# Optimization experiments

Hardware: AMD Instinct MI355X
Metric: run time of the kernel (lower is better)

The kernel has to match this reference:

```python
import jax, jax.numpy as jnp
import numpy as np


def setup_inputs() -> dict:
    key = jax.random.key(0)
    ks = jax.random.split(key, 7)
    IN, OUT, B = 8192, 8192, 256
    return {
        "x": jax.random.normal(ks[0], (B, IN), dtype=jnp.float32),
        "mu_weights": jax.random.normal(ks[1], (OUT, IN), dtype=jnp.float32) * 0.02,
        "rho_weights": jax.random.normal(ks[2], (OUT, IN), dtype=jnp.float32) * 0.1 - 3.0,
        "mu_bias": jax.random.normal(ks[3], (OUT,), dtype=jnp.float32) * 0.02,
        "rho_bias": jax.random.normal(ks[4], (OUT,), dtype=jnp.float32) * 0.1 - 3.0,
        "eps_w": jax.random.normal(ks[5], (OUT, IN), dtype=jnp.float32),
        "eps_b": jax.random.normal(ks[6], (OUT,), dtype=jnp.float32),
    }


def reference(x, mu_weights, rho_weights, mu_bias, rho_bias, eps_w, eps_b):
    # sigma = log(1 + exp(rho))  (softplus); W = mu + sigma * eps
    sigma_w = jnp.log1p(jnp.exp(rho_weights))
    W = mu_weights + sigma_w * eps_w            # [out, in]
    out = jnp.einsum("bi,oi->bo", x, W)          # x @ W.T -> [b, out]
    sigma_b = jnp.log1p(jnp.exp(rho_bias))
    b = mu_bias + sigma_b * eps_b                # [out]
    return out + b
```

## Files before the change

### kernel.cpp

```cpp
#include <hip/hip_runtime.h>

typedef _Float16 f16;
typedef _Float16 f16x8 __attribute__((ext_vector_type(8)));
typedef float f32x4 __attribute__((ext_vector_type(4)));

#define IN_DIM  8192
#define OUT_DIM 8192
#define BATCH   256
#define BK      32
#define BN      128
#define NSPLIT  4
#define KSPL    (IN_DIM / NSPLIT)
#define NSTEP   (KSPL / BK)

__device__ __forceinline__ float softplus_f(float r) {
    return __logf(1.0f + __expf(r));
}

#define ISSUE(S, A0a,A0b,A1a,A1b,M0,M1,R0,R1,E0,E1) do {                     \
    const int o_ = (S) * BK;                                                 \
    A0a = *(const f32x4*)(xp0 + o_);   A0b = *(const f32x4*)(xp0 + o_ + 4);  \
    A1a = *(const f32x4*)(xp1 + o_);   A1b = *(const f32x4*)(xp1 + o_ + 4);  \
    M0  = *(const f32x4*)(mup + o_);   M1  = *(const f32x4*)(mup + o_ + 4);  \
    R0  = *(const f32x4*)(rhp + o_);   R1  = *(const f32x4*)(rhp + o_ + 4);  \
    E0  = *(const f32x4*)(epp + o_);   E1  = *(const f32x4*)(epp + o_ + 4);  \
} while (0)

#define COMMIT(BUF, A0a,A0b,A1a,A1b,M0,M1,R0,R1,E0,E1) do {                  \
    f16x8 av0_, av1_, wv_;                                                   \
    _Pragma("unroll")                                                        \
    for (int q_ = 0; q_ < 4; ++q_) {                                         \
        av0_[q_]   = (f16)A0a[q_];  av0_[4+q_] = (f16)A0b[q_];               \
        av1_[q_]   = (f16)A1a[q_];  av1_[4+q_] = (f16)A1b[q_];               \
        wv_[q_]   = (f16)(M0[q_] + softplus_f(R0[q_]) * E0[q_]);             \
        wv_[4+q_] = (f16)(M1[q_] + softplus_f(R1[q_]) * E1[q_]);             \
    }                                                                        \
    *(f16x8*)&sm[BUF][a_st0] = av0_;                                         \
    *(f16x8*)&sm[BUF][a_st1] = av1_;                                         \
    *(f16x8*)&sm[BUF][b_st]  = wv_;                                          \
} while (0)

#define MSTEP(BUF) do {                                                      \
    f16x8 af_[4], bf_[4];                                                    \
    const int sl_ = lane >> 4;                                               \
    _Pragma("unroll")                                                        \
    for (int i_ = 0; i_ < 4; ++i_) {                                         \
        const int ar_ = wm * 64 + i_ * 16 + (lane & 15);                     \
        af_[i_] = *(const f16x8*)&sm[BUF][ar_ * BK + ((sl_ ^ (ar_ & 3)) << 3)]; \
        const int br_ = wn * 64 + i_ * 16 + (lane & 15);                     \
        bf_[i_] = *(const f16x8*)&sm[BUF][BATCH * BK + br_ * BK + ((sl_ ^ (br_ & 3)) << 3)]; \
    }                                                                        \
    _Pragma("unroll")                                                        \
    for (int i_ = 0; i_ < 4; ++i_)                                           \
        _Pragma("unroll")                                                    \
        for (int j_ = 0; j_ < 4; ++j_)                                       \
            acc[i_][j_] = __builtin_amdgcn_mfma_f32_16x16x32_f16(            \
                af_[i_], bf_[j_], acc[i_][j_], 0, 0, 0);                     \
} while (0)

#define BARRIER() do {                                                       \
    asm volatile("s_waitcnt lgkmcnt(0)" ::: "memory");                       \
    __builtin_amdgcn_s_barrier();                                            \
} while (0)

__global__ __launch_bounds__(512, 2)
void vl_main(const float* __restrict__ x,
             const float* __restrict__ muw,
             const float* __restrict__ rhow,
             const float* __restrict__ epsw,
             const float* __restrict__ mub,
             const float* __restrict__ rhob,
             const float* __restrict__ epsb,
             float* __restrict__ out)
{
    __shared__ __align__(16) f16 sm[2][BATCH * BK + BN * BK];

    const int t    = threadIdx.x;
    const int lane = t & 63;
    const int wid  = t >> 6;
    const int wm   = wid >> 1;
    const int wn   = wid & 1;

    const int bx = blockIdx.x;
    const int x7 = bx & 7;
    const int sk = x7 >> 1;
    const int nb = (x7 & 1) * 32 + (bx >> 3);
    const int k_base = sk * KSPL;
    const int n_base = nb * BN;

    const int slot = t & 3;
    const int row  = t >> 2;

    const float* xp0 = x + (size_t)row * IN_DIM + k_base + slot * 8;
    const float* xp1 = xp0 + (size_t)128 * IN_DIM;
    const size_t woff = (size_t)(n_base + row) * IN_DIM + k_base + slot * 8;
    const float* mup = muw  + woff;
    const float* rhp = rhow + woff;
    const float* epp = epsw + woff;

    const int a_sw  = (slot ^ (row & 3)) << 3;
    const int a_st0 = row * BK + a_sw;
    const int a_st1 = (row + 128) * BK + a_sw;
    const int b_st  = BATCH * BK + row * BK + a_sw;

    f32x4 acc[4][4];
#pragma unroll
    for (int i = 0; i < 4; ++i)
#pragma unroll
        for (int j = 0; j < 4; ++j)
            acc[i][j] = (f32x4){0.f, 0.f, 0.f, 0.f};

    f32x4 A0a0,A0b0,A1a0,A1b0,M00,M10,R00,R10,E00,E10;
    f32x4 A0a1,A0b1,A1a1,A1b1,M01,M11,R01,R11,E01,E11;

    ISSUE(0, A0a0,A0b0,A1a0,A1b0,M00,M10,R00,R10,E00,E10);
    ISSUE(1, A0a1,A0b1,A1a1,A1b1,M01,M11,R01,R11,E01,E11);
    COMMIT(0, A0a0,A0b0,A1a0,A1b0,M00,M10,R00,R10,E00,E10);
    BARRIER();

    for (int s = 0; s < NSTEP; s += 2) {
        if (s + 2 < NSTEP) ISSUE(s + 2, A0a0,A0b0,A1a0,A1b0,M00,M10,R00,R10,E00,E10);
        MSTEP(0);
        COMMIT(1, A0a1,A0b1,A1a1,A1b1,M01,M11,R01,R11,E01,E11);
        BARRIER();
        if (s + 3 < NSTEP) ISSUE(s + 3, A0a1,A0b1,A1a1,A1b1,M01,M11,R01,R11,E01,E11);
        MSTEP(1);
        if (s + 2 < NSTEP) COMMIT(0, A0a0,A0b0,A1a0,A1b0,M00,M10,R00,R10,E00,E10);
        BARRIER();
    }

    float bias[4] = {0.f, 0.f, 0.f, 0.f};
    if (sk == 0) {
#pragma unroll
        for (int j = 0; j < 4; ++j) {
            const int c = n_base + wn * 64 + j * 16 + (lane & 15);
            bias[j] = mub[c] + softplus_f(rhob[c]) * epsb[c];
        }
    }
#pragma unroll
    for (int i = 0; i < 4; ++i) {
        const int r = wm * 64 + i * 16 + ((lane >> 4) << 2);
#pragma unroll
        for (int j = 0; j < 4; ++j) {
            const int c = n_base + wn * 64 + j * 16 + (lane & 15);
            float* po = out + (size_t)r * OUT_DIM + c;
#pragma unroll
            for (int q = 0; q < 4; ++q)
                atomicAdd(po + (size_t)q * OUT_DIM, acc[i][j][q] + bias[j]);
        }
    }
}

extern "C" void kernel_launch(void* const* d_in, const int* in_sizes, int n_in,
                              void* d_out, int out_size, void* d_ws, size_t ws_size,
                              hipStream_t stream) {
    (void)in_sizes; (void)n_in; (void)d_ws; (void)ws_size;
    const float* x    = (const float*)d_in[0];
    const float* muw  = (const float*)d_in[1];
    const float* rhow = (const float*)d_in[2];
    const float* mub  = (const float*)d_in[3];
    const float* rhob = (const float*)d_in[4];
    const float* epsw = (const float*)d_in[5];
    const float* epsb = (const float*)d_in[6];
    float* out = (float*)d_out;

    hipMemsetAsync(out, 0, (size_t)out_size * sizeof(float), stream);
    vl_main<<<dim3(256), dim3(512), 0, stream>>>(x, muw, rhow, epsw,
                                                 mub, rhob, epsb, out);
}
```

Before: 214.0 us.

## Load x fragments directly into registers and keep only W in LDS

Activation tiles are no longer staged through shared memory. Each wave loads its x rows straight from global memory in MFMA fragment layout, converts them to fp16 in registers, and prefetches one step ahead. Shared memory now holds only the generated weight tile, with a new swizzle, and the last barrier of the loop is skipped. This is meant to cut LDS traffic, LDS footprint and barrier cost. In exchange, x is read redundantly by the two waves that share a row range, with less coalesced 32-byte segments per row, and register pressure goes up.

```diff
diff --git a/kernel.cpp b/kernel.cpp
--- a/kernel.cpp
+++ b/kernel.cpp
@@ -17,45 +17,56 @@
     return __logf(1.0f + __expf(r));
 }
 
-#define ISSUE(S, A0a,A0b,A1a,A1b,M0,M1,R0,R1,E0,E1) do {                     \
+#define ISSUE_W(S, Ma,Mb,Ra,Rb,Ea,Eb) do {                                   \
     const int o_ = (S) * BK;                                                 \
-    A0a = *(const f32x4*)(xp0 + o_);   A0b = *(const f32x4*)(xp0 + o_ + 4);  \
-    A1a = *(const f32x4*)(xp1 + o_);   A1b = *(const f32x4*)(xp1 + o_ + 4);  \
-    M0  = *(const f32x4*)(mup + o_);   M1  = *(const f32x4*)(mup + o_ + 4);  \
-    R0  = *(const f32x4*)(rhp + o_);   R1  = *(const f32x4*)(rhp + o_ + 4);  \
-    E0  = *(const f32x4*)(epp + o_);   E1  = *(const f32x4*)(epp + o_ + 4);  \
+    Ma = *(const f32x4*)(mup + o_);   Mb = *(const f32x4*)(mup + o_ + 4);    \
+    Ra = *(const f32x4*)(rhp + o_);   Rb = *(const f32x4*)(rhp + o_ + 4);    \
+    Ea = *(const f32x4*)(epp + o_);   Eb = *(const f32x4*)(epp + o_ + 4);    \
 } while (0)
 
-#define COMMIT(BUF, A0a,A0b,A1a,A1b,M0,M1,R0,R1,E0,E1) do {                  \
-    f16x8 av0_, av1_, wv_;                                                   \
+#define COMMIT_W(BUF, Ma,Mb,Ra,Rb,Ea,Eb) do {                                \
+    f16x8 wv_;                                                               \
     _Pragma("unroll")                                                        \
     for (int q_ = 0; q_ < 4; ++q_) {                                         \
-        av0_[q_]   = (f16)A0a[q_];  av0_[4+q_] = (f16)A0b[q_];               \
-        av1_[q_]   = (f16)A1a[q_];  av1_[4+q_] = (f16)A1b[q_];               \
-        wv_[q_]   = (f16)(M0[q_] + softplus_f(R0[q_]) * E0[q_]);             \
-        wv_[4+q_] = (f16)(M1[q_] + softplus_f(R1[q_]) * E1[q_]);             \
+        wv_[q_]   = (f16)(Ma[q_] + softplus_f(Ra[q_]) * Ea[q_]);             \
+        wv_[4+q_] = (f16)(Mb[q_] + softplus_f(Rb[q_]) * Eb[q_]);             \
     }                                                                        \
-    *(f16x8*)&sm[BUF][a_st0] = av0_;                                         \
-    *(f16x8*)&sm[BUF][a_st1] = av1_;                                         \
-    *(f16x8*)&sm[BUF][b_st]  = wv_;                                          \
+    *(f16x8*)&sm[BUF][b_st] = wv_;                                           \
+} while (0)
+
+#define ISSUE_A(S) do {                                                      \
+    const int o_ = (S) * BK;                                                 \
+    Ap0 = *(const f32x4*)(xa0 + o_);  Ap1 = *(const f32x4*)(xa0 + o_ + 4);   \
+    Ap2 = *(const f32x4*)(xa1 + o_);  Ap3 = *(const f32x4*)(xa1 + o_ + 4);   \
+    Ap4 = *(const f32x4*)(xa2 + o_);  Ap5 = *(const f32x4*)(xa2 + o_ + 4);   \
+    Ap6 = *(const f32x4*)(xa3 + o_);  Ap7 = *(const f32x4*)(xa3 + o_ + 4);   \
+} while (0)
+
+#define CVT_A() do {                                                         \
+    _Pragma("unroll")                                                        \
+    for (int q_ = 0; q_ < 4; ++q_) {                                         \
+        af0[q_] = (f16)Ap0[q_];  af0[4+q_] = (f16)Ap1[q_];                   \
+        af1[q_] = (f16)Ap2[q_];  af1[4+q_] = (f16)Ap3[q_];                   \
+        af2[q_] = (f16)Ap4[q_];  af2[4+q_] = (f16)Ap5[q_];                   \
+        af3[q_] = (f16)Ap6[q_];  af3[4+q_] = (f16)Ap7[q_];                   \
+    }                                                                        \
 } while (0)
 
 #define MSTEP(BUF) do {                                                      \
-    f16x8 af_[4], bf_[4];                                                    \
-    const int sl_ = lane >> 4;                                               \
+    f16x8 bf_[4];                                                            \
     _Pragma("unroll")                                                        \
-    for (int i_ = 0; i_ < 4; ++i_) {                                         \
-        const int ar_ = wm * 64 + i_ * 16 + (lane & 15);                     \
-        af_[i_] = *(const f16x8*)&sm[BUF][ar_ * BK + ((sl_ ^ (ar_ & 3)) << 3)]; \
-        const int br_ = wn * 64 + i_ * 16 + (lane & 15);                     \
-        bf_[i_] = *(const f16x8*)&sm[BUF][BATCH * BK + br_ * BK + ((sl_ ^ (br_ & 3)) << 3)]; \
+    for (int j_ = 0; j_ < 4; ++j_) {                                         \
+        const int br_ = wn * 64 + j_ * 16 + (lane & 15);                     \
+        bf_[j_] = *(const f16x8*)&sm[BUF][br_ * BK +                         \
+                    (((lane >> 4) ^ ((br_ >> 1) & 3)) << 3)];                \
     }                                                                        \
     _Pragma("unroll")                                                        \
-    for (int i_ = 0; i_ < 4; ++i_)                                           \
-        _Pragma("unroll")                                                    \
-        for (int j_ = 0; j_ < 4; ++j_)                                       \
-            acc[i_][j_] = __builtin_amdgcn_mfma_f32_16x16x32_f16(            \
-                af_[i_], bf_[j_], acc[i_][j_], 0, 0, 0);                     \
+    for (int j_ = 0; j_ < 4; ++j_) {                                         \
+        acc[0][j_] = __builtin_amdgcn_mfma_f32_16x16x32_f16(af0, bf_[j_], acc[0][j_], 0, 0, 0); \
+        acc[1][j_] = __builtin_amdgcn_mfma_f32_16x16x32_f16(af1, bf_[j_], acc[1][j_], 0, 0, 0); \
+        acc[2][j_] = __builtin_amdgcn_mfma_f32_16x16x32_f16(af2, bf_[j_], acc[2][j_], 0, 0, 0); \
+        acc[3][j_] = __builtin_amdgcn_mfma_f32_16x16x32_f16(af3, bf_[j_], acc[3][j_], 0, 0, 0); \
+    }                                                                        \
 } while (0)
 
 #define BARRIER() do {                                                       \
@@ -73,7 +84,7 @@
              const float* __restrict__ epsb,
              float* __restrict__ out)
 {
-    __shared__ __align__(16) f16 sm[2][BATCH * BK + BN * BK];
+    __shared__ __align__(16) f16 sm[2][BN * BK];
 
     const int t    = threadIdx.x;
     const int lane = t & 63;
@@ -90,18 +101,18 @@
 
     const int slot = t & 3;
     const int row  = t >> 2;
-
-    const float* xp0 = x + (size_t)row * IN_DIM + k_base + slot * 8;
-    const float* xp1 = xp0 + (size_t)128 * IN_DIM;
     const size_t woff = (size_t)(n_base + row) * IN_DIM + k_base + slot * 8;
     const float* mup = muw  + woff;
     const float* rhp = rhow + woff;
     const float* epp = epsw + woff;
 
-    const int a_sw  = (slot ^ (row & 3)) << 3;
-    const int a_st0 = row * BK + a_sw;
-    const int a_st1 = (row + 128) * BK + a_sw;
-    const int b_st  = BATCH * BK + row * BK + a_sw;
+    const int b_st = row * BK + ((slot ^ ((row >> 1) & 3)) << 3);
+
+    const int kf = (lane >> 4) * 8;
+    const float* xa0 = x + (size_t)(wm * 64 +  0 + (lane & 15)) * IN_DIM + k_base + kf;
+    const float* xa1 = x + (size_t)(wm * 64 + 16 + (lane & 15)) * IN_DIM + k_base + kf;
+    const float* xa2 = x + (size_t)(wm * 64 + 32 + (lane & 15)) * IN_DIM + k_base + kf;
+    const float* xa3 = x + (size_t)(wm * 64 + 48 + (lane & 15)) * IN_DIM + k_base + kf;
 
     f32x4 acc[4][4];
 #pragma unroll
@@ -110,23 +121,32 @@
         for (int j = 0; j < 4; ++j)
             acc[i][j] = (f32x4){0.f, 0.f, 0.f, 0.f};
 
-    f32x4 A0a0,A0b0,A1a0,A1b0,M00,M10,R00,R10,E00,E10;
-    f32x4 A0a1,A0b1,A1a1,A1b1,M01,M11,R01,R11,E01,E11;
+    f32x4 Ap0, Ap1, Ap2, Ap3, Ap4, Ap5, Ap6, Ap7;
+    f32x4 M0a, M0b, R0a, R0b, E0a, E0b;
+    f32x4 M1a, M1b, R1a, R1b, E1a, E1b;
+    f16x8 af0, af1, af2, af3;
 
-    ISSUE(0, A0a0,A0b0,A1a0,A1b0,M00,M10,R00,R10,E00,E10);
-    ISSUE(1, A0a1,A0b1,A1a1,A1b1,M01,M11,R01,R11,E01,E11);
-    COMMIT(0, A0a0,A0b0,A1a0,A1b0,M00,M10,R00,R10,E00,E10);
+    ISSUE_A(0);
+    ISSUE_W(0, M0a, M0b, R0a, R0b, E0a, E0b);
+    ISSUE_W(1, M1a, M1b, R1a, R1b, E1a, E1b);
+    COMMIT_W(0, M0a, M0b, R0a, R0b, E0a, E0b);
     BARRIER();
 
     for (int s = 0; s < NSTEP; s += 2) {
-        if (s + 2 < NSTEP) ISSUE(s + 2, A0a0,A0b0,A1a0,A1b0,M00,M10,R00,R10,E00,E10);
+        CVT_A();
+        ISSUE_A(s + 1);
+        if (s + 2 < NSTEP) ISSUE_W(s + 2, M0a, M0b, R0a, R0b, E0a, E0b);
         MSTEP(0);
-        COMMIT(1, A0a1,A0b1,A1a1,A1b1,M01,M11,R01,R11,E01,E11);
+        COMMIT_W(1, M1a, M1b, R1a, R1b, E1a, E1b);
         BARRIER();
-        if (s + 3 < NSTEP) ISSUE(s + 3, A0a1,A0b1,A1a1,A1b1,M01,M11,R01,R11,E01,E11);
+        CVT_A();
+        if (s + 2 < NSTEP) ISSUE_A(s + 2);
+        if (s + 3 < NSTEP) ISSUE_W(s + 3, M1a, M1b, R1a, R1b, E1a, E1b);
         MSTEP(1);
-        if (s + 2 < NSTEP) COMMIT(0, A0a0,A0b0,A1a0,A1b0,M00,M10,R00,R10,E00,E10);
-        BARRIER();
+        if (s + 2 < NSTEP) {
+            COMMIT_W(0, M0a, M0b, R0a, R0b, E0a, E0b);
+            BARRIER();
+        }
     }
 
     float bias[4] = {0.f, 0.f, 0.f, 0.f};
```

After: 259.5 us. +21.3%, slower.

## Deepen K-tile to 64 with inline-asm loads and manual vmcnt pipelining

Applied to the files above, without the earlier changes.

Doubles the K step per stage from 32 to 64 and issues global loads through inline `global_load_dwordx4` asm. Explicit `s_waitcnt vmcnt` and sched barriers control when the weight and activation registers are consumed, so the x and weight streams are prefetched a stage ahead. The x tile moves to a single-buffered LDS region with a wider XOR swizzle, while the weight tile stays double-buffered. The aim is to hide HBM latency better and halve the loop-iteration overhead, at the cost of more registers, extra barriers per iteration, and fragile hand-counted wait thresholds.

```diff
diff --git a/kernel.cpp b/kernel.cpp
--- a/kernel.cpp
+++ b/kernel.cpp
@@ -6,56 +6,83 @@
 
 #define IN_DIM  8192
 #define OUT_DIM 8192
-#define BATCH   256
-#define BK      32
-#define BN      128
 #define NSPLIT  4
 #define KSPL    (IN_DIM / NSPLIT)
-#define NSTEP   (KSPL / BK)
+#define BKM     64
+#define NM      (KSPL / BKM)
 
 __device__ __forceinline__ float softplus_f(float r) {
     return __logf(1.0f + __expf(r));
 }
 
-#define ISSUE(S, A0a,A0b,A1a,A1b,M0,M1,R0,R1,E0,E1) do {                     \
-    const int o_ = (S) * BK;                                                 \
-    A0a = *(const f32x4*)(xp0 + o_);   A0b = *(const f32x4*)(xp0 + o_ + 4);  \
-    A1a = *(const f32x4*)(xp1 + o_);   A1b = *(const f32x4*)(xp1 + o_ + 4);  \
-    M0  = *(const f32x4*)(mup + o_);   M1  = *(const f32x4*)(mup + o_ + 4);  \
-    R0  = *(const f32x4*)(rhp + o_);   R1  = *(const f32x4*)(rhp + o_ + 4);  \
-    E0  = *(const f32x4*)(epp + o_);   E1  = *(const f32x4*)(epp + o_ + 4);  \
-} while (0)
-
-#define COMMIT(BUF, A0a,A0b,A1a,A1b,M0,M1,R0,R1,E0,E1) do {                  \
-    f16x8 av0_, av1_, wv_;                                                   \
+#define GLD16(dst, p, LIT) \
+    asm volatile("global_load_dwordx4 %0, %1, off offset:" LIT \
+                 : "=&v"(dst) : "v"(p))
+
+#define SCHED0() __builtin_amdgcn_sched_barrier(0)
+
+#define ISSUE_W(M0,M1,M2,M3,R0,R1,R2,R3,E0,E1,E2,E3, S) do {                 \
+    const float* pm_ = mup + (size_t)(S) * BKM;                              \
+    const float* pr_ = rhp + (size_t)(S) * BKM;                              \
+    const float* pe_ = epp + (size_t)(S) * BKM;                              \
+    GLD16(M0, pm_, "0");  GLD16(M1, pm_, "16");                              \
+    GLD16(M2, pm_, "32"); GLD16(M3, pm_, "48");                              \
+    GLD16(R0, pr_, "0");  GLD16(R1, pr_, "16");                              \
+    GLD16(R2, pr_, "32"); GLD16(R3, pr_, "48");                              \
+    GLD16(E0, pe_, "0");  GLD16(E1, pe_, "16");                              \
+    GLD16(E2, pe_, "32"); GLD16(E3, pe_, "48");                              \
+} while (0)
+
+#define ISSUE_A(S) do {                                                      \
+    const float* pa_ = xap + (size_t)(S) * BKM;                              \
+    GLD16(Aa, pa_, "0");   GLD16(Ab, pa_, "16");                             \
+    GLD16(Ac, pa_, "32");  GLD16(Ad, pa_, "48");                             \
+    GLD16(Ae, pa_, "64");  GLD16(Af, pa_, "80");                             \
+    GLD16(Ag, pa_, "96");  GLD16(Ah, pa_, "112");                            \
+} while (0)
+
+#define COMMIT_W(BUF, M0,M1,M2,M3,R0,R1,R2,R3,E0,E1,E2,E3) do {              \
+    f16x8 w0_, w1_;                                                          \
     _Pragma("unroll")                                                        \
     for (int q_ = 0; q_ < 4; ++q_) {                                         \
-        av0_[q_]   = (f16)A0a[q_];  av0_[4+q_] = (f16)A0b[q_];               \
-        av1_[q_]   = (f16)A1a[q_];  av1_[4+q_] = (f16)A1b[q_];               \
-        wv_[q_]   = (f16)(M0[q_] + softplus_f(R0[q_]) * E0[q_]);             \
-        wv_[4+q_] = (f16)(M1[q_] + softplus_f(R1[q_]) * E1[q_]);             \
+        w0_[q_]   = (f16)(M0[q_] + softplus_f(R0[q_]) * E0[q_]);             \
+        w0_[4+q_] = (f16)(M1[q_] + softplus_f(R1[q_]) * E1[q_]);             \
+        w1_[q_]   = (f16)(M2[q_] + softplus_f(R2[q_]) * E2[q_]);             \
+        w1_[4+q_] = (f16)(M3[q_] + softplus_f(R3[q_]) * E3[q_]);             \
     }                                                                        \
-    *(f16x8*)&sm[BUF][a_st0] = av0_;                                         \
-    *(f16x8*)&sm[BUF][a_st1] = av1_;                                         \
-    *(f16x8*)&sm[BUF][b_st]  = wv_;                                          \
-} while (0)
-
-#define MSTEP(BUF) do {                                                      \
-    f16x8 af_[4], bf_[4];                                                    \
-    const int sl_ = lane >> 4;                                               \
+    *(f16x8*)&smW[BUF][ws0] = w0_;                                           \
+    *(f16x8*)&smW[BUF][ws1] = w1_;                                           \
+} while (0)
+
+#define COMMIT_A() do {                                                      \
+    f16x8 a0_, a1_, a2_, a3_;                                                \
+    _Pragma("unroll")                                                        \
+    for (int q_ = 0; q_ < 4; ++q_) {                                         \
+        a0_[q_] = (f16)Aa[q_];  a0_[4+q_] = (f16)Ab[q_];                     \
+        a1_[q_] = (f16)Ac[q_];  a1_[4+q_] = (f16)Ad[q_];                     \
+        a2_[q_] = (f16)Ae[q_];  a2_[4+q_] = (f16)Af[q_];                     \
+        a3_[q_] = (f16)Ag[q_];  a3_[4+q_] = (f16)Ah[q_];                     \
+    }                                                                        \
+    *(f16x8*)&smA[as0] = a0_;  *(f16x8*)&smA[as1] = a1_;                     \
+    *(f16x8*)&smA[as2] = a2_;  *(f16x8*)&smA[as3] = a3_;                     \
+} while (0)
+
+#define MSTEP(B, HH) do {                                                    \
+    const int ko_ = (HH) * 4 + (lane >> 4);                                  \
+    const int rr_ = lane & 15;                                               \
+    const int xw_ = (ko_ ^ (rr_ & 7)) << 3;                                  \
+    f16x8 bf_[4];                                                            \
+    _Pragma("unroll")                                                        \
+    for (int j_ = 0; j_ < 4; ++j_)                                           \
+        bf_[j_] = *(const f16x8*)&smW[B][(wn*64 + j_*16 + rr_)*BKM + xw_];   \
     _Pragma("unroll")                                                        \
     for (int i_ = 0; i_ < 4; ++i_) {                                         \
-        const int ar_ = wm * 64 + i_ * 16 + (lane & 15);                     \
-        af_[i_] = *(const f16x8*)&sm[BUF][ar_ * BK + ((sl_ ^ (ar_ & 3)) << 3)]; \
-        const int br_ = wn * 64 + i_ * 16 + (lane & 15);                     \
-        bf_[i_] = *(const f16x8*)&sm[BUF][BATCH * BK + br_ * BK + ((sl_ ^ (br_ & 3)) << 3)]; \
-    }                                                                        \
-    _Pragma("unroll")                                                        \
-    for (int i_ = 0; i_ < 4; ++i_)                                           \
+        const f16x8 af_ = *(const f16x8*)&smA[(wm*64 + i_*16 + rr_)*BKM + xw_]; \
         _Pragma("unroll")                                                    \
         for (int j_ = 0; j_ < 4; ++j_)                                       \
             acc[i_][j_] = __builtin_amdgcn_mfma_f32_16x16x32_f16(            \
-                af_[i_], bf_[j_], acc[i_][j_], 0, 0, 0);                     \
+                af_, bf_[j_], acc[i_][j_], 0, 0, 0);                         \
+    }                                                                        \
 } while (0)
 
 #define BARRIER() do {                                                       \
@@ -73,7 +100,8 @@
              const float* __restrict__ epsb,
              float* __restrict__ out)
 {
-    __shared__ __align__(16) f16 sm[2][BATCH * BK + BN * BK];
+    __shared__ __align__(16) f16 smA[256 * BKM];
+    __shared__ __align__(16) f16 smW[2][128 * BKM];
 
     const int t    = threadIdx.x;
     const int lane = t & 63;
@@ -86,22 +114,24 @@
     const int sk = x7 >> 1;
     const int nb = (x7 & 1) * 32 + (bx >> 3);
     const int k_base = sk * KSPL;
-    const int n_base = nb * BN;
+    const int n_base = nb * 128;
 
     const int slot = t & 3;
-    const int row  = t >> 2;
-
-    const float* xp0 = x + (size_t)row * IN_DIM + k_base + slot * 8;
-    const float* xp1 = xp0 + (size_t)128 * IN_DIM;
-    const size_t woff = (size_t)(n_base + row) * IN_DIM + k_base + slot * 8;
+    const int rw   = t >> 2;
+    const size_t woff = (size_t)(n_base + rw) * IN_DIM + k_base + slot * 16;
     const float* mup = muw  + woff;
     const float* rhp = rhow + woff;
     const float* epp = epsw + woff;
-
-    const int a_sw  = (slot ^ (row & 3)) << 3;
-    const int a_st0 = row * BK + a_sw;
-    const int a_st1 = (row + 128) * BK + a_sw;
-    const int b_st  = BATCH * BK + row * BK + a_sw;
+    const int ws0 = rw * BKM + (((2*slot + 0) ^ (rw & 7)) << 3);
+    const int ws1 = rw * BKM + (((2*slot + 1) ^ (rw & 7)) << 3);
+
+    const int ra = t >> 1;
+    const int ha = t & 1;
+    const float* xap = x + (size_t)ra * IN_DIM + k_base + ha * 32;
+    const int as0 = ra * BKM + (((ha*4 + 0) ^ (ra & 7)) << 3);
+    const int as1 = ra * BKM + (((ha*4 + 1) ^ (ra & 7)) << 3);
+    const int as2 = ra * BKM + (((ha*4 + 2) ^ (ra & 7)) << 3);
+    const int as3 = ra * BKM + (((ha*4 + 3) ^ (ra & 7)) << 3);
 
     f32x4 acc[4][4];
 #pragma unroll
@@ -110,24 +140,42 @@
         for (int j = 0; j < 4; ++j)
             acc[i][j] = (f32x4){0.f, 0.f, 0.f, 0.f};
 
-    f32x4 A0a0,A0b0,A1a0,A1b0,M00,M10,R00,R10,E00,E10;
-    f32x4 A0a1,A0b1,A1a1,A1b1,M01,M11,R01,R11,E01,E11;
-
-    ISSUE(0, A0a0,A0b0,A1a0,A1b0,M00,M10,R00,R10,E00,E10);
-    ISSUE(1, A0a1,A0b1,A1a1,A1b1,M01,M11,R01,R11,E01,E11);
-    COMMIT(0, A0a0,A0b0,A1a0,A1b0,M00,M10,R00,R10,E00,E10);
+    f32x4 Aa, Ab, Ac, Ad, Ae, Af, Ag, Ah;
+    f32x4 M00,M01,M02,M03, R00,R01,R02,R03, E00,E01,E02,E03;
+    f32x4 M10,M11,M12,M13, R10,R11,R12,R13, E10,E11,E12,E13;
+
+    ISSUE_W(M00,M01,M02,M03,R00,R01,R02,R03,E00,E01,E02,E03, 0);
+    ISSUE_A(0);
+    asm volatile("s_waitcnt vmcnt(0)"); SCHED0();
+    COMMIT_W(0, M00,M01,M02,M03,R00,R01,R02,R03,E00,E01,E02,E03);
+    COMMIT_A();
+    ISSUE_W(M00,M01,M02,M03,R00,R01,R02,R03,E00,E01,E02,E03, 1);
     BARRIER();
 
-    for (int s = 0; s < NSTEP; s += 2) {
-        if (s + 2 < NSTEP) ISSUE(s + 2, A0a0,A0b0,A1a0,A1b0,M00,M10,R00,R10,E00,E10);
-        MSTEP(0);
-        COMMIT(1, A0a1,A0b1,A1a1,A1b1,M01,M11,R01,R11,E01,E11);
-        BARRIER();
-        if (s + 3 < NSTEP) ISSUE(s + 3, A0a1,A0b1,A1a1,A1b1,M01,M11,R01,R11,E01,E11);
-        MSTEP(1);
-        if (s + 2 < NSTEP) COMMIT(0, A0a0,A0b0,A1a0,A1b0,M00,M10,R00,R10,E00,E10);
+    for (int s = 0; s < NM; s += 2) {
+        ISSUE_A(s + 1 < NM ? s + 1 : NM - 1);
+        ISSUE_W(M10,M11,M12,M13,R10,R11,R12,R13,E10,E11,E12,E13,
+                s + 2 < NM ? s + 2 : NM - 1);
+        MSTEP(0, 0); MSTEP(0, 1);
+        asm volatile("s_waitcnt vmcnt(20)"); SCHED0();
+        COMMIT_W(1, M00,M01,M02,M03,R00,R01,R02,R03,E00,E01,E02,E03);
+        BARRIER();
+        asm volatile("s_waitcnt vmcnt(12)"); SCHED0();
+        COMMIT_A();
+        BARRIER();
+
+        ISSUE_A(s + 2 < NM ? s + 2 : NM - 1);
+        ISSUE_W(M00,M01,M02,M03,R00,R01,R02,R03,E00,E01,E02,E03,
+                s + 3 < NM ? s + 3 : NM - 1);
+        MSTEP(1, 0); MSTEP(1, 1);
+        asm volatile("s_waitcnt vmcnt(20)"); SCHED0();
+        COMMIT_W(0, M10,M11,M12,M13,R10,R11,R12,R13,E10,E11,E12,E13);
+        BARRIER();
+        asm volatile("s_waitcnt vmcnt(12)"); SCHED0();
+        COMMIT_A();
         BARRIER();
     }
+    asm volatile("s_waitcnt vmcnt(0)" ::: "memory"); SCHED0();
 
     float bias[4] = {0.f, 0.f, 0.f, 0.f};
     if (sk == 0) {
```

New measurement: 245.6 us. +14.8%, slower.
